# Performance work log

Measured on AMD Instinct MI355X. Metric: run time of the kernel, lower is better.

Reference implementation:

```python
import jax, jax.numpy as jnp
import numpy as np

N_NODES = 100000
N_EDGES = 1600000
IN, HID, OUT = 128, 128, 64


def setup_inputs() -> dict:
    key = jax.random.key(0)
    ks = jax.random.split(key, 12)
    x = jax.random.normal(ks[0], (N_NODES, IN), dtype=jnp.float32)
    src = jax.random.randint(ks[1], (N_EDGES,), 0, N_NODES, dtype=jnp.int32)
    dst = jax.random.randint(ks[2], (N_EDGES,), 0, N_NODES, dtype=jnp.int32)
    def lin(k, fan_in, fan_out):
        s = 1.0 / np.sqrt(fan_in)
        return (jax.random.normal(k, (fan_in, fan_out), dtype=jnp.float32) * s)
    dims = [(IN, HID), (HID, HID), (HID, OUT)]
    params = {}
    for l, (fi, fo) in enumerate(dims):
        params[f"Wself{l}"] = lin(ks[3 + 3 * l], fi, fo)
        params[f"Wneigh{l}"] = lin(ks[4 + 3 * l], fi, fo)
        params[f"b{l}"] = jnp.zeros((fo,), dtype=jnp.float32)
    return {"x": x, "src": src, "dst": dst, **params}


def _sage_conv(h, src, dst, inv_deg, Ws, Wn, b):
    # mean aggregation over in-neighbors: segment-sum of gathered src feats / degree
    agg = jax.ops.segment_sum(h[src], dst, num_segments=N_NODES) * inv_deg
    return h @ Ws + agg @ Wn + b


def reference(x, src, dst, Wself0, Wneigh0, b0, Wself1, Wneigh1, b1, Wself2, Wneigh2, b2):
    deg = jax.ops.segment_sum(jnp.ones((N_EDGES,), jnp.float32), dst, num_segments=N_NODES)
    inv_deg = (1.0 / jnp.maximum(deg, 1.0))[:, None]  # zero-degree nodes get zero agg
    h = jax.nn.relu(_sage_conv(x, src, dst, inv_deg, Wself0, Wneigh0, b0))
    h = jax.nn.relu(_sage_conv(h, src, dst, inv_deg, Wself1, Wneigh1, b1))
    h = _sage_conv(h, src, dst, inv_deg, Wself2, Wneigh2, b2)
    return h
```

## Files before the change

kernel.cpp:

```cpp
#include <hip/hip_runtime.h>
#include <hip/hip_bf16.h>

#define N_NODES 100000
#define N_EDGES 1600000
#define BSHIFT 8
#define NB 391
#define BCAP 8192

typedef __attribute__((ext_vector_type(8))) short short8;
typedef __attribute__((ext_vector_type(4))) float f32x4;
typedef unsigned short ushort;
typedef unsigned int uint;

__device__ __forceinline__ ushort f2bf(float f) {
    uint u = __float_as_uint(f);
    uint r = (u + 0x7fffu + ((u >> 16) & 1u)) >> 16;
    return (ushort)r;
}
__device__ __forceinline__ float bflo(uint v) { return __uint_as_float(v << 16); }
__device__ __forceinline__ float bfhi(uint v) { return __uint_as_float(v & 0xffff0000u); }


__global__ __launch_bounds__(256) void partA_kernel(const int* __restrict__ src,
                                                    const int* __restrict__ dst,
                                                    uint* __restrict__ packed,
                                                    int* __restrict__ bucket_cnt, int E) {
    constexpr int PER = 16;
    __shared__ int cnt[NB];
    __shared__ int cur[NB];
    int tid = threadIdx.x;
    for (int i = tid; i < NB; i += 256) cnt[i] = 0;
    __syncthreads();
    int base = blockIdx.x * (256 * PER);
    int d[PER], s[PER];
#pragma unroll
    for (int i = 0; i < PER; i++) {
        int e = base + tid + i * 256;
        if (e < E) {
            d[i] = dst[e];
            s[i] = src[e];
            atomicAdd(&cnt[d[i] >> BSHIFT], 1);
        } else {
            d[i] = -1;
        }
    }
    __syncthreads();
    for (int i = tid; i < NB; i += 256) cur[i] = atomicAdd(&bucket_cnt[i], cnt[i]);
    __syncthreads();
#pragma unroll
    for (int i = 0; i < PER; i++) {
        if (d[i] >= 0) {
            int b = d[i] >> BSHIFT;
            int p = atomicAdd(&cur[b], 1);
            packed[(size_t)b * BCAP + p] = ((uint)(d[i] & 255) << 17) | (uint)s[i];
        }
    }
}


__global__ __launch_bounds__(512) void bscan_kernel(const int* __restrict__ bucket_cnt,
                                                    int* __restrict__ bucket_ofs) {
    __shared__ int s[512];
    int tid = threadIdx.x;
    int v = (tid < NB) ? bucket_cnt[tid] : 0;
    s[tid] = v;
    __syncthreads();
    for (int off = 1; off < 512; off <<= 1) {
        int x = s[tid];
        int y = (tid >= off) ? s[tid - off] : 0;
        __syncthreads();
        s[tid] = x + y;
        __syncthreads();
    }
    if (tid < NB) bucket_ofs[tid] = s[tid] - v;
}


__global__ __launch_bounds__(256) void partB_kernel(const uint* __restrict__ packed,
                                                    const int* __restrict__ bucket_cnt,
                                                    const int* __restrict__ bucket_ofs,
                                                    int* __restrict__ row_ptr,
                                                    float* __restrict__ inv_deg,
                                                    int* __restrict__ col, int N, int E) {
    __shared__ int deg[256];
    __shared__ int cur[256];
    __shared__ int psum[256];
    int b = blockIdx.x, tid = threadIdx.x;
    int cnt = bucket_cnt[b];
    int bofs = bucket_ofs[b];
    const uint* pk = packed + (size_t)b * BCAP;
    deg[tid] = 0;
    __syncthreads();
    for (int e = tid; e < cnt; e += 1024) {
        uint w[4];
        int have[4];
#pragma unroll
        for (int j = 0; j < 4; j++) {
            int ee = e + j * 256;
            have[j] = ee < cnt;
            w[j] = pk[have[j] ? ee : e];
        }
#pragma unroll
        for (int j = 0; j < 4; j++)
            if (have[j]) atomicAdd(&deg[w[j] >> 17], 1);
    }
    __syncthreads();
    int d0 = deg[tid];
    psum[tid] = d0;
    __syncthreads();
    for (int off = 1; off < 256; off <<= 1) {
        int x = psum[tid];
        int y = (tid >= off) ? psum[tid - off] : 0;
        __syncthreads();
        psum[tid] = x + y;
        __syncthreads();
    }
    int excl = psum[tid] - d0;
    cur[tid] = excl;
    int g = (b << BSHIFT) + tid;
    if (g < N) {
        row_ptr[g] = bofs + excl;
        inv_deg[g] = 1.0f / (float)(d0 > 1 ? d0 : 1);
    }
    if (b == 0 && tid == 0) row_ptr[N] = E;
    __syncthreads();
    for (int e = tid; e < cnt; e += 1024) {
        uint w[4];
        int have[4];
#pragma unroll
        for (int j = 0; j < 4; j++) {
            int ee = e + j * 256;
            have[j] = ee < cnt;
            w[j] = pk[have[j] ? ee : e];
        }
#pragma unroll
        for (int j = 0; j < 4; j++)
            if (have[j]) {
                int dl = w[j] >> 17;
                int p = atomicAdd(&cur[dl], 1);
                col[bofs + p] = (int)(w[j] & 0x1FFFFu);
            }
    }
}


__global__ __launch_bounds__(256) void cast_x_kernel(const float* __restrict__ x,
                                                     ushort* __restrict__ xb, long n8) {
    long g = (long)blockIdx.x * blockDim.x + threadIdx.x;
    if (g >= n8) return;
    const float4* x4 = (const float4*)x;
    float4 a = x4[g * 2], b = x4[g * 2 + 1];
    uint4 o;
    o.x = (uint)f2bf(a.x) | ((uint)f2bf(a.y) << 16);
    o.y = (uint)f2bf(a.z) | ((uint)f2bf(a.w) << 16);
    o.z = (uint)f2bf(b.x) | ((uint)f2bf(b.y) << 16);
    o.w = (uint)f2bf(b.z) | ((uint)f2bf(b.w) << 16);
    ((uint4*)xb)[g] = o;
}


__global__ void mk_bt_kernel(const float* __restrict__ Ws, const float* __restrict__ Wn,
                             ushort* __restrict__ BT, int FOUT) {
    int idx = blockIdx.x * blockDim.x + threadIdx.x;
    if (idx >= FOUT * 256) return;
    int n = idx >> 8, k = idx & 255;
    float v = (k < 128) ? Ws[k * FOUT + n] : Wn[(k - 128) * FOUT + n];
    BT[idx] = f2bf(v);
}


__global__ __launch_bounds__(256) void agg_kernel(const ushort* __restrict__ hb,
                                                  const int* __restrict__ row_ptr,
                                                  const int* __restrict__ col,
                                                  const float* __restrict__ inv_deg,
                                                  ushort* __restrict__ aggb, int n) {
    int node = (int)((blockIdx.x * blockDim.x + threadIdx.x) >> 6);
    int lane = threadIdx.x & 63;
    if (node >= n) return;
    int quad = lane >> 4;
    int sub = lane & 15;
    const char* hbase = (const char*)hb;
    int beg = row_ptr[node], end = row_ptr[node + 1];
    float acc[8];
#pragma unroll
    for (int j = 0; j < 8; j++) acc[j] = 0.f;
    int suboff = sub * 16;
    for (int e0 = beg; e0 < end; e0 += 8) {
        int rem = end - e0;
        int i0 = quad, i1 = quad + 4;
        float m0 = (i0 < rem) ? 1.f : 0.f;
        float m1 = (i1 < rem) ? 1.f : 0.f;
        int e0c = e0 + ((i0 < rem) ? i0 : 0);
        int e1c = e0 + ((i1 < rem) ? i1 : 0);
        int s0 = col[e0c], s1 = col[e1c];
        uint4 v0 = *(const uint4*)(hbase + (((uint)s0 << 8) + suboff));
        uint4 v1 = *(const uint4*)(hbase + (((uint)s1 << 8) + suboff));
        acc[0] += bflo(v0.x) * m0; acc[1] += bfhi(v0.x) * m0;
        acc[2] += bflo(v0.y) * m0; acc[3] += bfhi(v0.y) * m0;
        acc[4] += bflo(v0.z) * m0; acc[5] += bfhi(v0.z) * m0;
        acc[6] += bflo(v0.w) * m0; acc[7] += bfhi(v0.w) * m0;
        acc[0] += bflo(v1.x) * m1; acc[1] += bfhi(v1.x) * m1;
        acc[2] += bflo(v1.y) * m1; acc[3] += bfhi(v1.y) * m1;
        acc[4] += bflo(v1.z) * m1; acc[5] += bfhi(v1.z) * m1;
        acc[6] += bflo(v1.w) * m1; acc[7] += bfhi(v1.w) * m1;
    }
#pragma unroll
    for (int j = 0; j < 8; j++) {
        acc[j] += __shfl_xor(acc[j], 16);
        acc[j] += __shfl_xor(acc[j], 32);
    }
    if (quad == 0) {
        float inv = inv_deg[node];
        uint4 o;
        o.x = (uint)f2bf(acc[0] * inv) | ((uint)f2bf(acc[1] * inv) << 16);
        o.y = (uint)f2bf(acc[2] * inv) | ((uint)f2bf(acc[3] * inv) << 16);
        o.z = (uint)f2bf(acc[4] * inv) | ((uint)f2bf(acc[5] * inv) << 16);
        o.w = (uint)f2bf(acc[6] * inv) | ((uint)f2bf(acc[7] * inv) << 16);
        *(uint4*)((char*)aggb + (size_t)node * 256 + suboff) = o;
    }
}


template <int FOUT, bool RELU, bool OUTBF16>
__global__ __launch_bounds__(256) void mfma_gemm(const ushort* __restrict__ hb,
                                                 const ushort* __restrict__ aggb,
                                                 const ushort* __restrict__ BTb,
                                                 const float* __restrict__ bias,
                                                 void* __restrict__ outp, int nNodes) {
    constexpr int NT = FOUT / 16;
    constexpr int BSTR = 40;
    __shared__ ushort BT[FOUT * BSTR];
    int tid = threadIdx.x;
    int wave = tid >> 6, lane = tid & 63;
    int m = lane & 15, quad = lane >> 4;
    int r0 = blockIdx.x * 64 + wave * 16;
    int arow = r0 + m;
    if (arow >= nNodes) arow = nNodes - 1;
    const ushort* hrow = hb + (size_t)arow * 128;
    const ushort* grow = aggb + (size_t)arow * 128;

    f32x4 acc[NT];
#pragma unroll
    for (int t = 0; t < NT; t++) acc[t] = (f32x4){0.f, 0.f, 0.f, 0.f};

#pragma unroll
    for (int kc = 0; kc < 8; kc++) {
        __syncthreads();
        constexpr int UNITS = FOUT * 4;
#pragma unroll
        for (int u0 = 0; u0 < UNITS / 256; u0++) {
            int u = tid + u0 * 256;
            int n = u >> 2, ko = (u & 3) * 8;
            short8 v = *(const short8*)(BTb + n * 256 + kc * 32 + ko);
            *(short8*)(&BT[n * BSTR + ko]) = v;
        }
        __syncthreads();
        int kg = kc * 32 + quad * 8;
        const ushort* ap = (kg < 128) ? (hrow + kg) : (grow + (kg - 128));
        short8 afrag = *(const short8*)ap;
#pragma unroll
        for (int t = 0; t < NT; t++) {
            short8 bfrag = *(const short8*)(&BT[(t * 16 + m) * BSTR + quad * 8]);
            acc[t] = __builtin_amdgcn_mfma_f32_16x16x32_bf16(afrag, bfrag, acc[t], 0, 0, 0);
        }
    }

#pragma unroll
    for (int reg = 0; reg < 4; reg++) {
        int orow = r0 + quad * 4 + reg;
        if (orow < nNodes) {
#pragma unroll
            for (int t = 0; t < NT; t++) {
                int j = t * 16 + m;
                float v = acc[t][reg] + bias[j];
                if (RELU) v = fmaxf(v, 0.f);
                if (OUTBF16)
                    ((ushort*)outp)[(size_t)orow * FOUT + j] = f2bf(v);
                else
                    ((float*)outp)[(size_t)orow * FOUT + j] = v;
            }
        }
    }
}

extern "C" void kernel_launch(void* const* d_in, const int* in_sizes, int n_in,
                              void* d_out, int out_size, void* d_ws, size_t ws_size,
                              hipStream_t stream) {
    const float* x   = (const float*)d_in[0];
    const int* src   = (const int*)d_in[1];
    const int* dst   = (const int*)d_in[2];
    const float* Ws0 = (const float*)d_in[3];
    const float* Wn0 = (const float*)d_in[4];
    const float* b0  = (const float*)d_in[5];
    const float* Ws1 = (const float*)d_in[6];
    const float* Wn1 = (const float*)d_in[7];
    const float* b1  = (const float*)d_in[8];
    const float* Ws2 = (const float*)d_in[9];
    const float* Wn2 = (const float*)d_in[10];
    const float* b2  = (const float*)d_in[11];
    float* out = (float*)d_out;

    const int N = N_NODES, E = N_EDGES;

    char* p = (char*)d_ws;
    auto take = [&](size_t bytes) {
        void* r = (void*)p;
        p += (bytes + 255) & ~(size_t)255;
        return r;
    };
    uint* packed    = (uint*)take((size_t)NB * BCAP * 4);
    int* bucket_cnt = (int*)take((size_t)NB * 4);
    int* bucket_ofs = (int*)take((size_t)NB * 4);
    int* row_ptr    = (int*)take((size_t)(N + 1) * 4);
    int* col        = (int*)take((size_t)E * 4);
    float* inv_deg  = (float*)take((size_t)N * 4);
    ushort* xb      = (ushort*)take((size_t)N * 128 * 2);
    ushort* h1b     = (ushort*)take((size_t)N * 128 * 2);
    ushort* aggb    = (ushort*)take((size_t)N * 128 * 2);
    ushort* BT0     = (ushort*)take((size_t)128 * 256 * 2);
    ushort* BT1     = (ushort*)take((size_t)128 * 256 * 2);
    ushort* BT2     = (ushort*)take((size_t)64 * 256 * 2);

    hipMemsetAsync(bucket_cnt, 0, (size_t)NB * 4, stream);
    int nblkA = (E + 4096 - 1) / 4096;
    partA_kernel<<<nblkA, 256, 0, stream>>>(src, dst, packed, bucket_cnt, E);
    bscan_kernel<<<1, 512, 0, stream>>>(bucket_cnt, bucket_ofs);
    partB_kernel<<<NB, 256, 0, stream>>>(packed, bucket_cnt, bucket_ofs, row_ptr, inv_deg, col, N, E);

    long n8 = (long)N * 128 / 8;
    cast_x_kernel<<<(int)((n8 + 255) / 256), 256, 0, stream>>>(x, xb, n8);
    mk_bt_kernel<<<(128 * 256 + 255) / 256, 256, 0, stream>>>(Ws0, Wn0, BT0, 128);
    mk_bt_kernel<<<(128 * 256 + 255) / 256, 256, 0, stream>>>(Ws1, Wn1, BT1, 128);
    mk_bt_kernel<<<(64 * 256 + 255) / 256, 256, 0, stream>>>(Ws2, Wn2, BT2, 64);

    int aggGrid = (int)(((long)N * 64 + 255) / 256);
    int gemmGrid = (N + 63) / 64;

    agg_kernel<<<aggGrid, 256, 0, stream>>>(xb, row_ptr, col, inv_deg, aggb, N);
    mfma_gemm<128, true, true><<<gemmGrid, 256, 0, stream>>>(xb, aggb, BT0, b0, h1b, N);
    agg_kernel<<<aggGrid, 256, 0, stream>>>(h1b, row_ptr, col, inv_deg, aggb, N);
    mfma_gemm<128, true, true><<<gemmGrid, 256, 0, stream>>>(h1b, aggb, BT1, b1, xb, N);
    agg_kernel<<<aggGrid, 256, 0, stream>>>(xb, row_ptr, col, inv_deg, aggb, N);
    mfma_gemm<64, false, false><<<gemmGrid, 256, 0, stream>>>(xb, aggb, BT2, b2, out, N);
}
```

Baseline: 402.4 us.

## Fold bucket scan into partB, merge prep kernels, widen agg gather unroll

Removes the single-block bucket scan kernel by having each partB block compute its own bucket offset as a block reduction over the preceding bucket counts. The x cast and the three weight-transpose kernels become one launch, cutting four launches down to one. The aggregation loop now handles 16 edges per iteration with four independent gathers per lane, giving more memory-level parallelism. The cost is redundant prefix work across the 391 partB blocks and more masked wasted loads for low-degree nodes.

```diff
diff --git a/kernel.cpp b/kernel.cpp
--- a/kernel.cpp
+++ b/kernel.cpp
@@ -58,36 +58,30 @@
 }
 
 
-__global__ __launch_bounds__(512) void bscan_kernel(const int* __restrict__ bucket_cnt,
-                                                    int* __restrict__ bucket_ofs) {
-    __shared__ int s[512];
-    int tid = threadIdx.x;
-    int v = (tid < NB) ? bucket_cnt[tid] : 0;
-    s[tid] = v;
-    __syncthreads();
-    for (int off = 1; off < 512; off <<= 1) {
-        int x = s[tid];
-        int y = (tid >= off) ? s[tid - off] : 0;
-        __syncthreads();
-        s[tid] = x + y;
-        __syncthreads();
-    }
-    if (tid < NB) bucket_ofs[tid] = s[tid] - v;
-}
-
-
 __global__ __launch_bounds__(256) void partB_kernel(const uint* __restrict__ packed,
                                                     const int* __restrict__ bucket_cnt,
-                                                    const int* __restrict__ bucket_ofs,
                                                     int* __restrict__ row_ptr,
                                                     float* __restrict__ inv_deg,
                                                     int* __restrict__ col, int N, int E) {
     __shared__ int deg[256];
     __shared__ int cur[256];
     __shared__ int psum[256];
+    __shared__ int sofs;
     int b = blockIdx.x, tid = threadIdx.x;
     int cnt = bucket_cnt[b];
-    int bofs = bucket_ofs[b];
+    {
+        int part = 0;
+        for (int i = tid; i < b; i += 256) part += bucket_cnt[i];
+        psum[tid] = part;
+        __syncthreads();
+        for (int off = 128; off > 0; off >>= 1) {
+            if (tid < off) psum[tid] += psum[tid + off];
+            __syncthreads();
+        }
+        if (tid == 0) sofs = psum[0];
+        __syncthreads();
+    }
+    int bofs = sofs;
     const uint* pk = packed + (size_t)b * BCAP;
     deg[tid] = 0;
     __syncthreads();
@@ -144,25 +138,50 @@
 }
 
 
-__global__ __launch_bounds__(256) void cast_x_kernel(const float* __restrict__ x,
-                                                     ushort* __restrict__ xb, long n8) {
-    long g = (long)blockIdx.x * blockDim.x + threadIdx.x;
-    if (g >= n8) return;
-    const float4* x4 = (const float4*)x;
-    float4 a = x4[g * 2], b = x4[g * 2 + 1];
-    uint4 o;
-    o.x = (uint)f2bf(a.x) | ((uint)f2bf(a.y) << 16);
-    o.y = (uint)f2bf(a.z) | ((uint)f2bf(a.w) << 16);
-    o.z = (uint)f2bf(b.x) | ((uint)f2bf(b.y) << 16);
-    o.w = (uint)f2bf(b.z) | ((uint)f2bf(b.w) << 16);
-    ((uint4*)xb)[g] = o;
-}
-
-
-__global__ void mk_bt_kernel(const float* __restrict__ Ws, const float* __restrict__ Wn,
-                             ushort* __restrict__ BT, int FOUT) {
-    int idx = blockIdx.x * blockDim.x + threadIdx.x;
-    if (idx >= FOUT * 256) return;
+#define CAST_BLK 6250
+
+__global__ __launch_bounds__(256) void prep_kernel(const float* __restrict__ x,
+                                                   ushort* __restrict__ xb,
+                                                   const float* __restrict__ Ws0,
+                                                   const float* __restrict__ Wn0,
+                                                   const float* __restrict__ Ws1,
+                                                   const float* __restrict__ Wn1,
+                                                   const float* __restrict__ Ws2,
+                                                   const float* __restrict__ Wn2,
+                                                   ushort* __restrict__ BT0,
+                                                   ushort* __restrict__ BT1,
+                                                   ushort* __restrict__ BT2) {
+    int blk = blockIdx.x;
+    if (blk < CAST_BLK) {
+        long n8 = (long)N_NODES * 128 / 8;
+        long g = (long)blk * 256 + threadIdx.x;
+        if (g >= n8) return;
+        const float4* x4 = (const float4*)x;
+        float4 a = x4[g * 2], b = x4[g * 2 + 1];
+        uint4 o;
+        o.x = (uint)f2bf(a.x) | ((uint)f2bf(a.y) << 16);
+        o.y = (uint)f2bf(a.z) | ((uint)f2bf(a.w) << 16);
+        o.z = (uint)f2bf(b.x) | ((uint)f2bf(b.y) << 16);
+        o.w = (uint)f2bf(b.z) | ((uint)f2bf(b.w) << 16);
+        ((uint4*)xb)[g] = o;
+        return;
+    }
+    int idx = (blk - CAST_BLK) * 256 + threadIdx.x;
+    const float* Ws;
+    const float* Wn;
+    ushort* BT;
+    int FOUT;
+    if (idx < 128 * 256) {
+        Ws = Ws0; Wn = Wn0; BT = BT0; FOUT = 128;
+    } else if (idx < 2 * 128 * 256) {
+        idx -= 128 * 256;
+        Ws = Ws1; Wn = Wn1; BT = BT1; FOUT = 128;
+    } else if (idx < 2 * 128 * 256 + 64 * 256) {
+        idx -= 2 * 128 * 256;
+        Ws = Ws2; Wn = Wn2; BT = BT2; FOUT = 64;
+    } else {
+        return;
+    }
     int n = idx >> 8, k = idx & 255;
     float v = (k < 128) ? Ws[k * FOUT + n] : Wn[(k - 128) * FOUT + n];
     BT[idx] = f2bf(v);
@@ -185,24 +204,27 @@
 #pragma unroll
     for (int j = 0; j < 8; j++) acc[j] = 0.f;
     int suboff = sub * 16;
-    for (int e0 = beg; e0 < end; e0 += 8) {
+    for (int e0 = beg; e0 < end; e0 += 16) {
         int rem = end - e0;
-        int i0 = quad, i1 = quad + 4;
-        float m0 = (i0 < rem) ? 1.f : 0.f;
-        float m1 = (i1 < rem) ? 1.f : 0.f;
-        int e0c = e0 + ((i0 < rem) ? i0 : 0);
-        int e1c = e0 + ((i1 < rem) ? i1 : 0);
-        int s0 = col[e0c], s1 = col[e1c];
-        uint4 v0 = *(const uint4*)(hbase + (((uint)s0 << 8) + suboff));
-        uint4 v1 = *(const uint4*)(hbase + (((uint)s1 << 8) + suboff));
-        acc[0] += bflo(v0.x) * m0; acc[1] += bfhi(v0.x) * m0;
-        acc[2] += bflo(v0.y) * m0; acc[3] += bfhi(v0.y) * m0;
-        acc[4] += bflo(v0.z) * m0; acc[5] += bfhi(v0.z) * m0;
-        acc[6] += bflo(v0.w) * m0; acc[7] += bfhi(v0.w) * m0;
-        acc[0] += bflo(v1.x) * m1; acc[1] += bfhi(v1.x) * m1;
-        acc[2] += bflo(v1.y) * m1; acc[3] += bfhi(v1.y) * m1;
-        acc[4] += bflo(v1.z) * m1; acc[5] += bfhi(v1.z) * m1;
-        acc[6] += bflo(v1.w) * m1; acc[7] += bfhi(v1.w) * m1;
+        int idxv[4];
+        float msk[4];
+#pragma unroll
+        for (int j = 0; j < 4; j++) {
+            int i = quad + 4 * j;
+            msk[j] = (i < rem) ? 1.f : 0.f;
+            idxv[j] = col[e0 + ((i < rem) ? i : 0)];
+        }
+        uint4 v[4];
+#pragma unroll
+        for (int j = 0; j < 4; j++)
+            v[j] = *(const uint4*)(hbase + (((uint)idxv[j] << 8) + suboff));
+#pragma unroll
+        for (int j = 0; j < 4; j++) {
+            acc[0] += bflo(v[j].x) * msk[j]; acc[1] += bfhi(v[j].x) * msk[j];
+            acc[2] += bflo(v[j].y) * msk[j]; acc[3] += bfhi(v[j].y) * msk[j];
+            acc[4] += bflo(v[j].z) * msk[j]; acc[5] += bfhi(v[j].z) * msk[j];
+            acc[6] += bflo(v[j].w) * msk[j]; acc[7] += bfhi(v[j].w) * msk[j];
+        }
     }
 #pragma unroll
     for (int j = 0; j < 8; j++) {
@@ -310,7 +332,6 @@
     };
     uint* packed    = (uint*)take((size_t)NB * BCAP * 4);
     int* bucket_cnt = (int*)take((size_t)NB * 4);
-    int* bucket_ofs = (int*)take((size_t)NB * 4);
     int* row_ptr    = (int*)take((size_t)(N + 1) * 4);
     int* col        = (int*)take((size_t)E * 4);
     float* inv_deg  = (float*)take((size_t)N * 4);
@@ -324,14 +345,10 @@
     hipMemsetAsync(bucket_cnt, 0, (size_t)NB * 4, stream);
     int nblkA = (E + 4096 - 1) / 4096;
     partA_kernel<<<nblkA, 256, 0, stream>>>(src, dst, packed, bucket_cnt, E);
-    bscan_kernel<<<1, 512, 0, stream>>>(bucket_cnt, bucket_ofs);
-    partB_kernel<<<NB, 256, 0, stream>>>(packed, bucket_cnt, bucket_ofs, row_ptr, inv_deg, col, N, E);
-
-    long n8 = (long)N * 128 / 8;
-    cast_x_kernel<<<(int)((n8 + 255) / 256), 256, 0, stream>>>(x, xb, n8);
-    mk_bt_kernel<<<(128 * 256 + 255) / 256, 256, 0, stream>>>(Ws0, Wn0, BT0, 128);
-    mk_bt_kernel<<<(128 * 256 + 255) / 256, 256, 0, stream>>>(Ws1, Wn1, BT1, 128);
-    mk_bt_kernel<<<(64 * 256 + 255) / 256, 256, 0, stream>>>(Ws2, Wn2, BT2, 64);
+    partB_kernel<<<NB, 256, 0, stream>>>(packed, bucket_cnt, row_ptr, inv_deg, col, N, E);
+
+    prep_kernel<<<CAST_BLK + 320, 256, 0, stream>>>(x, xb, Ws0, Wn0, Ws1, Wn1, Ws2, Wn2,
+                                                    BT0, BT1, BT2);
 
     int aggGrid = (int)(((long)N * 64 + 255) / 256);
     int gemmGrid = (N + 63) / 64;
```

Result: faster. 389.8 us (-3.1%).
